# Optimization experiments

Hardware: AMD Instinct MI355X
Metric: run time of the kernel (lower is better)

Reference implementation:

```python
import jax, jax.numpy as jnp
import numpy as np

N_TOKENS = 4096   # flattened batch*seq tokens
D_MODEL = 1024
N_EXPERT = 8
D_HIDDEN = 1024   # expert FFN hidden size
TOP_K = 2


def setup_inputs() -> dict:
    key = jax.random.key(0)
    ks = jax.random.split(key, 4)
    f32 = jnp.float32
    return {
        "inp": jax.random.normal(ks[0], (N_TOKENS, D_MODEL), f32),
        "gate_w": jax.random.normal(ks[1], (D_MODEL, N_EXPERT), f32) * 0.02,
        "gate_b": jnp.zeros((N_EXPERT,), f32),
        "w1": jax.random.normal(ks[2], (N_EXPERT, D_MODEL, D_HIDDEN), f32) * 0.02,
        "b1": jnp.zeros((N_EXPERT, D_HIDDEN), f32),
        "w2": jax.random.normal(ks[3], (N_EXPERT, D_HIDDEN, D_MODEL), f32) * 0.02,
        "b2": jnp.zeros((N_EXPERT, D_MODEL), f32),
    }


def reference(inp, gate_w, gate_b, w1, b1, w2, b2):
    """FMoE forward: NaiveGate top-k -> dispatch -> per-expert FFN -> weighted combine.

    Math is identical to dispatch/grouped-GEMM/gather: since both top-k slots of a
    token see the same input, out[n] = sum_e coeff[n,e] * expert_e(inp[n]) where
    coeff[n,e] = sum_k softmax(top_vals)[n,k] * 1[top_idx[n,k] == e].
    """
    n_expert = gate_w.shape[-1]
    # NaiveGate: linear gate, top-k, softmax over the k selected logits
    logits = inp @ gate_w + gate_b                      # [N, E]
    top_val, top_idx = jax.lax.top_k(logits, TOP_K)     # [N, K]
    score = jax.nn.softmax(top_val, axis=-1)            # [N, K]
    # combine weights per (token, expert); top-k indices are distinct per token
    coeff = jnp.sum(
        jax.nn.one_hot(top_idx, n_expert, dtype=inp.dtype) * score[..., None],
        axis=1,
    )                                                   # [N, E]
    # expert FFN (exact-erf GeLU, matching torch.nn.functional.gelu)
    h = jax.nn.gelu(jnp.einsum('nd,edh->neh', inp, w1) + b1, approximate=False)  # [N, E, H]
    out = jnp.einsum('neh,ehd->nd', h * coeff[:, :, None], w2) + coeff @ b2      # [N, D]
    return out


if __name__ == "__main__":
    out = reference(**setup_inputs())
    print(out.shape, out.dtype)
```

## Files before the change

### kernel.cpp

```cpp
#include <hip/hip_runtime.h>
#include <math.h>

#define N_TOKENS 4096
#define D_MODEL  1024
#define N_EXPERT 8
#define D_HIDDEN 1024
#define N_POS    8192

typedef __bf16 bf16x8 __attribute__((ext_vector_type(8)));
typedef float  f32x4  __attribute__((ext_vector_type(4)));
typedef unsigned short u16x8 __attribute__((ext_vector_type(8)));

#define GLOBAL_AS __attribute__((address_space(1)))
#define LDS_AS    __attribute__((address_space(3)))

static __device__ __forceinline__ void async_ld16(const void* g, void* l) {
    __builtin_amdgcn_global_load_lds((GLOBAL_AS void*)g, (LDS_AS void*)l, 16, 0, 0);
}

static __device__ __forceinline__ unsigned short f2bf(float f) {
    unsigned int u = __builtin_bit_cast(unsigned int, f);
    u += 0x7fffu + ((u >> 16) & 1u);
    return (unsigned short)(u >> 16);
}
static __device__ __forceinline__ unsigned int pack2(float a, float b) {
    return (unsigned int)f2bf(a) | ((unsigned int)f2bf(b) << 16);
}

__global__ __launch_bounds__(256) void convert_transpose_kernel(
    const float* __restrict__ w1, const float* __restrict__ w2,
    unsigned short* __restrict__ w1b, unsigned short* __restrict__ w2b)
{
    int mat = blockIdx.z;
    const float* src = (mat < 8) ? (w1 + (size_t)mat * 1048576)
                                 : (w2 + (size_t)(mat - 8) * 1048576);
    unsigned short* dst = (mat < 8) ? (w1b + (size_t)mat * 1048576)
                                    : (w2b + (size_t)(mat - 8) * 1048576);
    __shared__ float tile[64][68];
    int r0 = blockIdx.x * 64, c0 = blockIdx.y * 64;
    int tid = threadIdx.x;
    #pragma unroll
    for (int i = 0; i < 4; ++i) {
        int r = (tid >> 4) + i * 16;
        float4 v = *(const float4*)(src + (size_t)(r0 + r) * 1024 + c0 + (tid & 15) * 4);
        *(float4*)&tile[r][(tid & 15) * 4] = v;
    }
    __syncthreads();
    #pragma unroll
    for (int i = 0; i < 2; ++i) {
        int dr = (tid & 31) + i * 32;
        int dc = (tid >> 5) * 8;
        u16x8 o;
        #pragma unroll
        for (int j = 0; j < 8; ++j) o[j] = f2bf(tile[dc + j][dr]);
        *(u16x8*)(dst + (size_t)(c0 + dr) * 1024 + r0 + dc) = o;
    }
}

__global__ __launch_bounds__(256) void gate_kernel(
    const float* __restrict__ inp, const float* __restrict__ gate_w,
    const float* __restrict__ gate_b, int* __restrict__ cnts,
    int* __restrict__ emeta, float* __restrict__ stok)
{
    __shared__ int bcnt[8], base[8];
    __shared__ int tinfo[16];
    int tid = threadIdx.x, lane = tid & 63, wave = tid >> 6;
    if (tid < 8) bcnt[tid] = 0;
    __syncthreads();

    for (int t = 0; t < 4; ++t) {
        int ti = wave * 4 + t;
        int n  = blockIdx.x * 16 + ti;
        const float* ip = inp + (size_t)n * D_MODEL;
        float acc[8] = {0.f,0.f,0.f,0.f,0.f,0.f,0.f,0.f};
        for (int d0 = lane * 4; d0 < D_MODEL; d0 += 256) {
            float4 x = *(const float4*)(ip + d0);
            #pragma unroll
            for (int j = 0; j < 4; ++j) {
                float xv = (j == 0) ? x.x : (j == 1) ? x.y : (j == 2) ? x.z : x.w;
                float4 g0 = *(const float4*)(gate_w + (d0 + j) * 8);
                float4 g1 = *(const float4*)(gate_w + (d0 + j) * 8 + 4);
                acc[0] += xv * g0.x; acc[1] += xv * g0.y;
                acc[2] += xv * g0.z; acc[3] += xv * g0.w;
                acc[4] += xv * g1.x; acc[5] += xv * g1.y;
                acc[6] += xv * g1.z; acc[7] += xv * g1.w;
            }
        }
        #pragma unroll
        for (int off = 32; off > 0; off >>= 1)
            #pragma unroll
            for (int e = 0; e < 8; ++e)
                acc[e] += __shfl_xor(acc[e], off, 64);
        #pragma unroll
        for (int e = 0; e < 8; ++e) acc[e] += gate_b[e];

        int e0 = 0; float v0 = acc[0];
        #pragma unroll
        for (int e = 1; e < 8; ++e) if (acc[e] > v0) { v0 = acc[e]; e0 = e; }
        int e1 = -1; float v1 = -1e30f;
        #pragma unroll
        for (int e = 0; e < 8; ++e) if (e != e0 && acc[e] > v1) { v1 = acc[e]; e1 = e; }
        float tv = expf(v1 - v0);
        float s0 = 1.0f / (1.0f + tv);
        float s1 = tv / (1.0f + tv);

        if (lane == 0) {
            int r0 = atomicAdd(&bcnt[e0], 1);
            int r1 = atomicAdd(&bcnt[e1], 1);
            tinfo[ti] = e0 | (e1 << 4) | (r0 << 8) | (r1 << 20);
            stok[2 * n]     = s0;
            stok[2 * n + 1] = s1;
        }
    }
    __syncthreads();
    if (tid < 8) base[tid] = atomicAdd(&cnts[tid], bcnt[tid]);
    __syncthreads();
    if (tid < 16) {
        int n = blockIdx.x * 16 + tid;
        unsigned int inf = (unsigned int)tinfo[tid];
        int e0 = inf & 15, e1 = (inf >> 4) & 15;
        int p0 = base[e0] + ((inf >> 8) & 4095);
        int p1 = base[e1] + (int)(inf >> 20);
        emeta[n] = e0 | (e1 << 4) | (p0 << 8) | (p1 << 20);
    }
}

__global__ __launch_bounds__(256) void gather_kernel(
    const float* __restrict__ inp, const int* __restrict__ cnts,
    const int* __restrict__ emeta, const float* __restrict__ stok,
    unsigned short* __restrict__ Ag, int* __restrict__ pos2tok,
    float* __restrict__ pos2score)
{
    int lane = threadIdx.x & 63, wave = threadIdx.x >> 6;
    int n = blockIdx.x * 4 + wave;
    unsigned int em = (unsigned int)emeta[n];
    int e0 = em & 15, e1 = (em >> 4) & 15;
    int p0 = (em >> 8) & 4095, p1 = (int)(em >> 20);
    int off0 = 0, off1 = 0;
    #pragma unroll
    for (int e = 0; e < 8; ++e) {
        int c = cnts[e];
        off0 += (e < e0) ? c : 0;
        off1 += (e < e1) ? c : 0;
    }
    int pos0 = off0 + p0, pos1 = off1 + p1;
    if (lane == 0) {
        pos2tok[pos0] = n;          pos2tok[pos1] = n;
        pos2score[pos0] = stok[2*n]; pos2score[pos1] = stok[2*n+1];
    }
    const float* ip = inp + (size_t)n * D_MODEL;
    unsigned short* r0 = Ag + (size_t)pos0 * D_MODEL;
    unsigned short* r1 = Ag + (size_t)pos1 * D_MODEL;
    for (int d = lane * 4; d < D_MODEL; d += 256) {
        float4 v = *(const float4*)(ip + d);
        uint2 u; u.x = pack2(v.x, v.y); u.y = pack2(v.z, v.w);
        *(uint2*)(r0 + d) = u;
        *(uint2*)(r1 + d) = u;
    }
}

__global__ __launch_bounds__(256) void out_init_kernel(
    const int* __restrict__ emeta, const float* __restrict__ stok,
    const float* __restrict__ b2, float* __restrict__ out)
{
    int lane = threadIdx.x & 63, wave = threadIdx.x >> 6;
    int n = blockIdx.x * 4 + wave;
    unsigned int em = (unsigned int)emeta[n];
    int e0 = em & 15, e1 = (em >> 4) & 15;
    float s0 = stok[2 * n], s1 = stok[2 * n + 1];
    const float* bA = b2 + (size_t)e0 * D_MODEL;
    const float* bB = b2 + (size_t)e1 * D_MODEL;
    float* op = out + (size_t)n * D_MODEL;
    for (int d = lane * 4; d < D_MODEL; d += 256) {
        float4 xa = *(const float4*)(bA + d);
        float4 xb = *(const float4*)(bB + d);
        float4 r;
        r.x = s0 * xa.x + s1 * xb.x; r.y = s0 * xa.y + s1 * xb.y;
        r.z = s0 * xa.z + s1 * xb.z; r.w = s0 * xa.w + s1 * xb.w;
        *(float4*)(op + d) = r;
    }
}

__global__ __launch_bounds__(256, 2) void ffn1_kernel(
    const unsigned short* __restrict__ Ag, const unsigned short* __restrict__ w1b,
    const float* __restrict__ b1, const int* __restrict__ cnts,
    unsigned short* __restrict__ Hg)
{
    int bid = blockIdx.x;
    int e = bid & 7, nt = (bid >> 3) & 7, mt = bid >> 6;
    int off = 0, Ne = 0;
    #pragma unroll
    for (int i = 0; i < 8; ++i) {
        int c = cnts[i];
        off += (i < e) ? c : 0;
        Ne = (i == e) ? c : Ne;
    }
    int m0 = mt * 128;
    if (m0 >= Ne) return;
    int n0 = nt * 128;

    __shared__ unsigned short As[2 * 128 * 32];
    __shared__ unsigned short Bs[2 * 128 * 32];

    int tid = threadIdx.x, lane = tid & 63, wave = tid >> 6;
    int lrow = lane >> 2, lchunk = lane & 3;
    int csw8 = (lchunk ^ ((lrow >> 1) & 3)) * 8;

    int ga0 = off + m0 + wave * 32 + lrow;
    int ga1 = ga0 + 16;
    if (ga0 >= N_POS) ga0 = N_POS - 1;
    if (ga1 >= N_POS) ga1 = N_POS - 1;
    const unsigned short* aS0 = Ag + (size_t)ga0 * D_MODEL + csw8;
    const unsigned short* aS1 = Ag + (size_t)ga1 * D_MODEL + csw8;
    const unsigned short* bS0 = w1b + (size_t)e * D_MODEL * D_HIDDEN
                              + (size_t)(n0 + wave * 32 + lrow) * D_MODEL + csw8;
    const unsigned short* bS1 = bS0 + (size_t)16 * D_MODEL;
    unsigned short* aD0 = &As[(wave * 32) * 32];
    unsigned short* aD1 = &As[(wave * 32 + 16) * 32];
    unsigned short* bD0 = &Bs[(wave * 32) * 32];
    unsigned short* bD1 = &Bs[(wave * 32 + 16) * 32];

    f32x4 acc[4][4] = {};
    int wm = (wave & 1) * 64, wn = (wave >> 1) * 64;
    int lane15 = lane & 15, quad = lane >> 4;
    int fro = (quad ^ ((lane15 >> 1) & 3)) * 8;

    for (int k0 = 0; k0 < D_MODEL; k0 += 64) {
        #pragma unroll
        for (int h = 0; h < 2; ++h) {
            int ko = k0 + h * 32;
            async_ld16(aS0 + ko, aD0 + h * 4096);
            async_ld16(aS1 + ko, aD1 + h * 4096);
            async_ld16(bS0 + ko, bD0 + h * 4096);
            async_ld16(bS1 + ko, bD1 + h * 4096);
        }
        __syncthreads();
        bf16x8 af[2][4], bf[2][4];
        #pragma unroll
        for (int h = 0; h < 2; ++h)
            #pragma unroll
            for (int t = 0; t < 4; ++t) {
                af[h][t] = *(const bf16x8*)&As[h * 4096 + (wm + t * 16 + lane15) * 32 + fro];
                bf[h][t] = *(const bf16x8*)&Bs[h * 4096 + (wn + t * 16 + lane15) * 32 + fro];
            }
        #pragma unroll
        for (int h = 0; h < 2; ++h)
            #pragma unroll
            for (int i = 0; i < 4; ++i)
                #pragma unroll
                for (int j = 0; j < 4; ++j)
                    acc[i][j] = __builtin_amdgcn_mfma_f32_16x16x32_bf16(
                        af[h][i], bf[h][j], acc[i][j], 0, 0, 0);
        __syncthreads();
    }

    const float* bexp = b1 + (size_t)e * D_HIDDEN;
    #pragma unroll
    for (int j = 0; j < 4; ++j) {
        int gcol = n0 + wn + j * 16 + lane15;
        float bv = bexp[gcol];
        #pragma unroll
        for (int i = 0; i < 4; ++i) {
            int rowb = wm + i * 16 + quad * 4;
            #pragma unroll
            for (int r = 0; r < 4; ++r) {
                int row = rowb + r;
                if (m0 + row < Ne) {
                    float x = acc[i][j][r] + bv;
                    float gv = 0.5f * x * (1.0f + erff(x * 0.70710678118654752f));
                    Hg[(size_t)(off + m0 + row) * D_HIDDEN + gcol] = f2bf(gv);
                }
            }
        }
    }
}

__global__ __launch_bounds__(256, 2) void ffn2_kernel(
    const unsigned short* __restrict__ Hg, const unsigned short* __restrict__ w2b,
    const int* __restrict__ cnts, const int* __restrict__ pos2tok,
    const float* __restrict__ pos2score, float* __restrict__ out)
{
    int bid = blockIdx.x;
    int e = bid & 7, nt = (bid >> 3) & 7, mt = bid >> 6;
    int off = 0, Ne = 0;
    #pragma unroll
    for (int i = 0; i < 8; ++i) {
        int c = cnts[i];
        off += (i < e) ? c : 0;
        Ne = (i == e) ? c : Ne;
    }
    int m0 = mt * 128;
    if (m0 >= Ne) return;
    int n0 = nt * 128;

    __shared__ unsigned short As[2 * 128 * 32];
    __shared__ unsigned short Bs[2 * 128 * 32];
    __shared__ int   ptok[128];
    __shared__ float psc[128];

    int tid = threadIdx.x, lane = tid & 63, wave = tid >> 6;
    int lrow = lane >> 2, lchunk = lane & 3;
    int csw8 = (lchunk ^ ((lrow >> 1) & 3)) * 8;

    int ga0 = off + m0 + wave * 32 + lrow;
    int ga1 = ga0 + 16;
    if (ga0 >= N_POS) ga0 = N_POS - 1;
    if (ga1 >= N_POS) ga1 = N_POS - 1;
    const unsigned short* aS0 = Hg + (size_t)ga0 * D_HIDDEN + csw8;
    const unsigned short* aS1 = Hg + (size_t)ga1 * D_HIDDEN + csw8;
    const unsigned short* bS0 = w2b + (size_t)e * D_HIDDEN * D_MODEL
                              + (size_t)(n0 + wave * 32 + lrow) * D_HIDDEN + csw8;
    const unsigned short* bS1 = bS0 + (size_t)16 * D_HIDDEN;
    unsigned short* aD0 = &As[(wave * 32) * 32];
    unsigned short* aD1 = &As[(wave * 32 + 16) * 32];
    unsigned short* bD0 = &Bs[(wave * 32) * 32];
    unsigned short* bD1 = &Bs[(wave * 32 + 16) * 32];

    f32x4 acc[4][4] = {};
    int wm = (wave & 1) * 64, wn = (wave >> 1) * 64;
    int lane15 = lane & 15, quad = lane >> 4;
    int fro = (quad ^ ((lane15 >> 1) & 3)) * 8;

    for (int k0 = 0; k0 < D_HIDDEN; k0 += 64) {
        #pragma unroll
        for (int h = 0; h < 2; ++h) {
            int ko = k0 + h * 32;
            async_ld16(aS0 + ko, aD0 + h * 4096);
            async_ld16(aS1 + ko, aD1 + h * 4096);
            async_ld16(bS0 + ko, bD0 + h * 4096);
            async_ld16(bS1 + ko, bD1 + h * 4096);
        }
        __syncthreads();
        bf16x8 af[2][4], bf[2][4];
        #pragma unroll
        for (int h = 0; h < 2; ++h)
            #pragma unroll
            for (int t = 0; t < 4; ++t) {
                af[h][t] = *(const bf16x8*)&As[h * 4096 + (wm + t * 16 + lane15) * 32 + fro];
                bf[h][t] = *(const bf16x8*)&Bs[h * 4096 + (wn + t * 16 + lane15) * 32 + fro];
            }
        #pragma unroll
        for (int h = 0; h < 2; ++h)
            #pragma unroll
            for (int i = 0; i < 4; ++i)
                #pragma unroll
                for (int j = 0; j < 4; ++j)
                    acc[i][j] = __builtin_amdgcn_mfma_f32_16x16x32_bf16(
                        af[h][i], bf[h][j], acc[i][j], 0, 0, 0);
        __syncthreads();
    }

    if (tid < 128) {
        int pos = off + m0 + tid;
        if (pos > N_POS - 1) pos = N_POS - 1;
        ptok[tid] = pos2tok[pos];
        psc[tid]  = pos2score[pos];
    }
    __syncthreads();

    #pragma unroll
    for (int j = 0; j < 4; ++j) {
        int gcol = n0 + wn + j * 16 + lane15;
        #pragma unroll
        for (int i = 0; i < 4; ++i) {
            int rowb = wm + i * 16 + quad * 4;
            #pragma unroll
            for (int r = 0; r < 4; ++r) {
                int row = rowb + r;
                if (m0 + row < Ne) {
                    atomicAdd(&out[(size_t)ptok[row] * D_MODEL + gcol],
                              psc[row] * acc[i][j][r]);
                }
            }
        }
    }
}

extern "C" void kernel_launch(void* const* d_in, const int* in_sizes, int n_in,
                              void* d_out, int out_size, void* d_ws, size_t ws_size,
                              hipStream_t stream) {
    const float* inp    = (const float*)d_in[0];
    const float* gate_w = (const float*)d_in[1];
    const float* gate_b = (const float*)d_in[2];
    const float* w1     = (const float*)d_in[3];
    const float* b1     = (const float*)d_in[4];
    const float* w2     = (const float*)d_in[5];
    const float* b2     = (const float*)d_in[6];
    float* out = (float*)d_out;

    char* ws = (char*)d_ws;
    unsigned short* w1b = (unsigned short*)(ws);
    unsigned short* w2b = (unsigned short*)(ws + 16777216);
    unsigned short* Hg  = (unsigned short*)(ws + 33554432);
    int*   cnts    = (int*)  (ws + 50331648);
    int*   emeta   = (int*)  (ws + 50331776);
    float* stok    = (float*)(ws + 50348160);
    int*   pos2tok = (int*)  (ws + 50380928);
    float* pos2sc  = (float*)(ws + 50413696);

    unsigned short* Ag = (unsigned short*)d_out;

    hipMemsetAsync(cnts, 0, N_EXPERT * sizeof(int), stream);
    convert_transpose_kernel<<<dim3(16, 16, 16), 256, 0, stream>>>(w1, w2, w1b, w2b);
    gate_kernel<<<dim3(N_TOKENS / 16), 256, 0, stream>>>(
        inp, gate_w, gate_b, cnts, emeta, stok);
    gather_kernel<<<dim3(N_TOKENS / 4), 256, 0, stream>>>(
        inp, cnts, emeta, stok, Ag, pos2tok, pos2sc);
    ffn1_kernel<<<dim3(2048), 256, 0, stream>>>(Ag, w1b, b1, cnts, Hg);
    out_init_kernel<<<dim3(N_TOKENS / 4), 256, 0, stream>>>(emeta, stok, b2, out);
    ffn2_kernel<<<dim3(2048), 256, 0, stream>>>(Hg, w2b, cnts, pos2tok, pos2sc, out);
}
```

Before: 252.1 us.

## Replace FFN2 scattered float atomics with bf16 staging plus per-token combine kernel

FFN2 now writes its per-position results as bf16 into a staging buffer, which reuses the w1b workspace region once FFN1 is done. It no longer scatters score-weighted float atomicAdds into the output. A new combine kernel gathers each token's two expert rows through a tok2pos map and adds the biases and gate scores. This replaces out_init and removes atomic contention and the extra output initialization pass. In exchange the staging round trip adds memory traffic, and FFN2 outputs are rounded to bf16 before the combine. The transpose kernel's write pattern is also remapped so each thread writes contiguous 16-byte chunks along a destination row.

```diff
diff --git a/kernel.cpp b/kernel.cpp
--- a/kernel.cpp
+++ b/kernel.cpp
@@ -25,6 +25,12 @@
 }
 static __device__ __forceinline__ unsigned int pack2(float a, float b) {
     return (unsigned int)f2bf(a) | ((unsigned int)f2bf(b) << 16);
+}
+static __device__ __forceinline__ float bflo(unsigned int u) {
+    return __builtin_bit_cast(float, u << 16);
+}
+static __device__ __forceinline__ float bfhi(unsigned int u) {
+    return __builtin_bit_cast(float, u & 0xffff0000u);
 }
 
 __global__ __launch_bounds__(256) void convert_transpose_kernel(
@@ -46,14 +52,14 @@
         *(float4*)&tile[r][(tid & 15) * 4] = v;
     }
     __syncthreads();
-    #pragma unroll
-    for (int i = 0; i < 2; ++i) {
-        int dr = (tid & 31) + i * 32;
-        int dc = (tid >> 5) * 8;
+    int dr = tid >> 2;
+    #pragma unroll
+    for (int p = 0; p < 2; ++p) {
+        int ch = (tid & 3) + p * 4;
         u16x8 o;
         #pragma unroll
-        for (int j = 0; j < 8; ++j) o[j] = f2bf(tile[dc + j][dr]);
-        *(u16x8*)(dst + (size_t)(c0 + dr) * 1024 + r0 + dc) = o;
+        for (int j = 0; j < 8; ++j) o[j] = f2bf(tile[ch * 8 + j][dr]);
+        *(u16x8*)(dst + (size_t)(c0 + dr) * 1024 + r0 + ch * 8) = o;
     }
 }
 
@@ -127,9 +133,8 @@
 
 __global__ __launch_bounds__(256) void gather_kernel(
     const float* __restrict__ inp, const int* __restrict__ cnts,
-    const int* __restrict__ emeta, const float* __restrict__ stok,
-    unsigned short* __restrict__ Ag, int* __restrict__ pos2tok,
-    float* __restrict__ pos2score)
+    const int* __restrict__ emeta, unsigned short* __restrict__ Ag,
+    int* __restrict__ tok2pos)
 {
     int lane = threadIdx.x & 63, wave = threadIdx.x >> 6;
     int n = blockIdx.x * 4 + wave;
@@ -145,8 +150,8 @@
     }
     int pos0 = off0 + p0, pos1 = off1 + p1;
     if (lane == 0) {
-        pos2tok[pos0] = n;          pos2tok[pos1] = n;
-        pos2score[pos0] = stok[2*n]; pos2score[pos1] = stok[2*n+1];
+        tok2pos[2 * n]     = pos0;
+        tok2pos[2 * n + 1] = pos1;
     }
     const float* ip = inp + (size_t)n * D_MODEL;
     unsigned short* r0 = Ag + (size_t)pos0 * D_MODEL;
@@ -156,28 +161,6 @@
         uint2 u; u.x = pack2(v.x, v.y); u.y = pack2(v.z, v.w);
         *(uint2*)(r0 + d) = u;
         *(uint2*)(r1 + d) = u;
-    }
-}
-
-__global__ __launch_bounds__(256) void out_init_kernel(
-    const int* __restrict__ emeta, const float* __restrict__ stok,
-    const float* __restrict__ b2, float* __restrict__ out)
-{
-    int lane = threadIdx.x & 63, wave = threadIdx.x >> 6;
-    int n = blockIdx.x * 4 + wave;
-    unsigned int em = (unsigned int)emeta[n];
-    int e0 = em & 15, e1 = (em >> 4) & 15;
-    float s0 = stok[2 * n], s1 = stok[2 * n + 1];
-    const float* bA = b2 + (size_t)e0 * D_MODEL;
-    const float* bB = b2 + (size_t)e1 * D_MODEL;
-    float* op = out + (size_t)n * D_MODEL;
-    for (int d = lane * 4; d < D_MODEL; d += 256) {
-        float4 xa = *(const float4*)(bA + d);
-        float4 xb = *(const float4*)(bB + d);
-        float4 r;
-        r.x = s0 * xa.x + s1 * xb.x; r.y = s0 * xa.y + s1 * xb.y;
-        r.z = s0 * xa.z + s1 * xb.z; r.w = s0 * xa.w + s1 * xb.w;
-        *(float4*)(op + d) = r;
     }
 }
 
@@ -277,8 +260,7 @@
 
 __global__ __launch_bounds__(256, 2) void ffn2_kernel(
     const unsigned short* __restrict__ Hg, const unsigned short* __restrict__ w2b,
-    const int* __restrict__ cnts, const int* __restrict__ pos2tok,
-    const float* __restrict__ pos2score, float* __restrict__ out)
+    const int* __restrict__ cnts, unsigned short* __restrict__ Og)
 {
     int bid = blockIdx.x;
     int e = bid & 7, nt = (bid >> 3) & 7, mt = bid >> 6;
@@ -295,8 +277,6 @@
 
     __shared__ unsigned short As[2 * 128 * 32];
     __shared__ unsigned short Bs[2 * 128 * 32];
-    __shared__ int   ptok[128];
-    __shared__ float psc[128];
 
     int tid = threadIdx.x, lane = tid & 63, wave = tid >> 6;
     int lrow = lane >> 2, lchunk = lane & 3;
@@ -350,14 +330,6 @@
         __syncthreads();
     }
 
-    if (tid < 128) {
-        int pos = off + m0 + tid;
-        if (pos > N_POS - 1) pos = N_POS - 1;
-        ptok[tid] = pos2tok[pos];
-        psc[tid]  = pos2score[pos];
-    }
-    __syncthreads();
-
     #pragma unroll
     for (int j = 0; j < 4; ++j) {
         int gcol = n0 + wn + j * 16 + lane15;
@@ -368,11 +340,41 @@
             for (int r = 0; r < 4; ++r) {
                 int row = rowb + r;
                 if (m0 + row < Ne) {
-                    atomicAdd(&out[(size_t)ptok[row] * D_MODEL + gcol],
-                              psc[row] * acc[i][j][r]);
+                    Og[(size_t)(off + m0 + row) * D_MODEL + gcol] =
+                        f2bf(acc[i][j][r]);
                 }
             }
         }
+    }
+}
+
+__global__ __launch_bounds__(256) void combine_kernel(
+    const unsigned short* __restrict__ Og, const int* __restrict__ tok2pos,
+    const float* __restrict__ stok, const int* __restrict__ emeta,
+    const float* __restrict__ b2, float* __restrict__ out)
+{
+    int lane = threadIdx.x & 63, wave = threadIdx.x >> 6;
+    int n = blockIdx.x * 4 + wave;
+    int pos0 = tok2pos[2 * n], pos1 = tok2pos[2 * n + 1];
+    float s0 = stok[2 * n], s1 = stok[2 * n + 1];
+    unsigned int em = (unsigned int)emeta[n];
+    int e0 = em & 15, e1 = (em >> 4) & 15;
+    const unsigned short* o0 = Og + (size_t)pos0 * D_MODEL;
+    const unsigned short* o1 = Og + (size_t)pos1 * D_MODEL;
+    const float* bA = b2 + (size_t)e0 * D_MODEL;
+    const float* bB = b2 + (size_t)e1 * D_MODEL;
+    float* op = out + (size_t)n * D_MODEL;
+    for (int d = lane * 4; d < D_MODEL; d += 256) {
+        uint2 u0 = *(const uint2*)(o0 + d);
+        uint2 u1 = *(const uint2*)(o1 + d);
+        float4 xa = *(const float4*)(bA + d);
+        float4 xb = *(const float4*)(bB + d);
+        float4 r;
+        r.x = s0 * (bflo(u0.x) + xa.x) + s1 * (bflo(u1.x) + xb.x);
+        r.y = s0 * (bfhi(u0.x) + xa.y) + s1 * (bfhi(u1.x) + xb.y);
+        r.z = s0 * (bflo(u0.y) + xa.z) + s1 * (bflo(u1.y) + xb.z);
+        r.w = s0 * (bfhi(u0.y) + xa.w) + s1 * (bfhi(u1.y) + xb.w);
+        *(float4*)(op + d) = r;
     }
 }
 
@@ -389,14 +391,14 @@
     float* out = (float*)d_out;
 
     char* ws = (char*)d_ws;
-    unsigned short* w1b = (unsigned short*)(ws);
-    unsigned short* w2b = (unsigned short*)(ws + 16777216);
-    unsigned short* Hg  = (unsigned short*)(ws + 33554432);
-    int*   cnts    = (int*)  (ws + 50331648);
-    int*   emeta   = (int*)  (ws + 50331776);
-    float* stok    = (float*)(ws + 50348160);
-    int*   pos2tok = (int*)  (ws + 50380928);
-    float* pos2sc  = (float*)(ws + 50413696);
+    int*   cnts    = (int*)  (ws);
+    int*   emeta   = (int*)  (ws + 4096);
+    float* stok    = (float*)(ws + 65536);
+    int*   tok2pos = (int*)  (ws + 131072);
+    unsigned short* w2b = (unsigned short*)(ws + 1048576);
+    unsigned short* Hg  = (unsigned short*)(ws + 17825792);
+    unsigned short* w1b = (unsigned short*)(ws + 34603008);
+    unsigned short* Og  = (unsigned short*)(ws + 34603008);
 
     unsigned short* Ag = (unsigned short*)d_out;
 
@@ -405,8 +407,9 @@
     gate_kernel<<<dim3(N_TOKENS / 16), 256, 0, stream>>>(
         inp, gate_w, gate_b, cnts, emeta, stok);
     gather_kernel<<<dim3(N_TOKENS / 4), 256, 0, stream>>>(
-        inp, cnts, emeta, stok, Ag, pos2tok, pos2sc);
+        inp, cnts, emeta, Ag, tok2pos);
     ffn1_kernel<<<dim3(2048), 256, 0, stream>>>(Ag, w1b, b1, cnts, Hg);
-    out_init_kernel<<<dim3(N_TOKENS / 4), 256, 0, stream>>>(emeta, stok, b2, out);
-    ffn2_kernel<<<dim3(2048), 256, 0, stream>>>(Hg, w2b, cnts, pos2tok, pos2sc, out);
-}
+    ffn2_kernel<<<dim3(2048), 256, 0, stream>>>(Hg, w2b, cnts, Og);
+    combine_kernel<<<dim3(N_TOKENS / 4), 256, 0, stream>>>(
+        Og, tok2pos, stok, emeta, b2, out);
+}
```

Measured after the change: 227.7 us. 1.11x faster.
